# Performance work log

Measured on AMD Instinct MI355X. Metric: run time of the kernel, lower is better.

Reference implementation:

```python
import jax, jax.numpy as jnp
import numpy as np

B, S, R = 1, 512, 384
C_MSA, C_Z, C_HID, N_HEAD = 64, 128, 32, 8
INF = 1e8


def layer_norm(x, gamma, beta, eps=1e-5):
    mu = jnp.mean(x, axis=-1, keepdims=True)
    var = jnp.mean(jnp.square(x - mu), axis=-1, keepdims=True)
    return (x - mu) * jax.lax.rsqrt(var + eps) * gamma + beta


def setup_inputs() -> dict:
    key = jax.random.key(0)
    ks = jax.random.split(key, 8)
    hc = N_HEAD * C_HID
    return {
        "m": jax.random.normal(ks[0], (B, S, R, C_MSA), jnp.float32),
        "z": jax.random.normal(ks[1], (B, R, R, C_Z), jnp.float32),
        "msa_mask": jnp.ones((B, S, R), jnp.float32),
        "z_mask": jnp.ones((B, R, R), jnp.float32),
        "ln_m_g": jnp.ones((C_MSA,), jnp.float32),
        "ln_m_b": jnp.zeros((C_MSA,), jnp.float32),
        "w_v": jax.random.normal(ks[2], (C_MSA, hc), jnp.float32) / np.sqrt(C_MSA),
        "w_g": jax.random.normal(ks[3], (C_MSA, hc), jnp.float32) * 0.02,
        "ln_z_g": jnp.ones((C_Z,), jnp.float32),
        "ln_z_b": jnp.zeros((C_Z,), jnp.float32),
        "w_b": jax.random.normal(ks[4], (C_Z, N_HEAD), jnp.float32) / np.sqrt(C_Z),
        "w_o": jax.random.normal(ks[5], (hc, C_MSA), jnp.float32) * 0.02,
    }


def reference(m, z, msa_mask, z_mask, ln_m_g, ln_m_b, w_v, w_g, ln_z_g, ln_z_b, w_b, w_o):
    b_, s_, r_ = m.shape[0], m.shape[1], m.shape[2]
    m_ln = layer_norm(m, ln_m_g, ln_m_b)                       # [B,S,R,Cm]
    v = (m_ln @ w_v).reshape(b_, s_, r_, N_HEAD, C_HID)        # [B,S,R,H,C]
    g = jax.nn.sigmoid(m_ln @ w_g).reshape(b_, s_, r_, N_HEAD, C_HID)
    bias = layer_norm(z, ln_z_g, ln_z_b) @ w_b                 # [B,R,R,H]
    bias = bias + INF * (z_mask[..., None] - 1.0)
    v = v * msa_mask[..., None, None]
    w = jax.nn.softmax(bias, axis=2)                           # softmax over j
    # weighted average over residues j, then sigmoid gating
    o = g * jnp.einsum('bijh,bsjhc->bsihc', w, v)              # [B,S,R,H,C]
    o = o.reshape(b_, s_, r_, N_HEAD * C_HID)
    return o @ w_o                                             # [B,S,R,Cm]
```

## Files before the change

### kernel.cpp

```cpp
#include <hip/hip_runtime.h>
#include <math.h>

#define S_DIM 512
#define R_DIM 384
#define CM 64
#define CZ 128
#define NH 8
#define CH 32
#define HC 256

typedef unsigned short u16;
typedef __attribute__((ext_vector_type(8))) __bf16 bf16x8;
typedef __attribute__((ext_vector_type(4))) float f32x4;

static __device__ __forceinline__ u16 f2bf(float f) {
    unsigned int u = __float_as_uint(f);
    unsigned int r = (u + 0x7fffu + ((u >> 16) & 1u)) >> 16;
    return (u16)r;
}
static __device__ __forceinline__ float bf2f(u16 h) {
    return __uint_as_float(((unsigned int)h) << 16);
}
static __device__ __forceinline__ void split2(float f, u16& hi, u16& lo) {
    hi = f2bf(f);
    lo = f2bf(f - bf2f(hi));
}

__global__ __launch_bounds__(256) void kW_prep(
    const float* __restrict__ wv, const float* __restrict__ wg,
    u16* __restrict__ wvT_hi, u16* __restrict__ wvT_lo,
    u16* __restrict__ wgT_hi, u16* __restrict__ wgT_lo)
{
    const int idx = blockIdx.x * 256 + threadIdx.x;
    const int which = idx >> 14;
    const int r = idx & 16383;
    const int n = r >> 6, c = r & 63;
    if (which == 0) split2(wv[c * HC + n], wvT_hi[r], wvT_lo[r]);
    else            split2(wg[c * HC + n], wgT_hi[r], wgT_lo[r]);
}

__global__ __launch_bounds__(256) void kA1_bias(
    const float* __restrict__ z, const float* __restrict__ z_mask,
    const float* __restrict__ ln_z_g, const float* __restrict__ ln_z_b,
    const float* __restrict__ w_b, float* __restrict__ bias_ws)
{
    __shared__ float wb_s[CZ * NH];
    __shared__ float zn_s[4][CZ];
    const int tid = threadIdx.x, w = tid >> 6, lane = tid & 63;
    const int ridx = blockIdx.x * 4 + w;

    #pragma unroll
    for (int q = 0; q < 4; ++q) wb_s[tid * 4 + q] = w_b[tid * 4 + q];

    const float2 zz = *reinterpret_cast<const float2*>(
        z + (size_t)ridx * CZ + lane * 2);
    float s1 = zz.x + zz.y;
    float s2 = zz.x * zz.x + zz.y * zz.y;
    #pragma unroll
    for (int msk = 32; msk >= 1; msk >>= 1) {
        s1 += __shfl_xor(s1, msk);
        s2 += __shfl_xor(s2, msk);
    }
    const float mu   = s1 * (1.0f / CZ);
    const float var  = s2 * (1.0f / CZ) - mu * mu;
    const float rstd = rsqrtf(var + 1e-5f);
    const int c0 = lane * 2;
    zn_s[w][c0]     = (zz.x - mu) * rstd * ln_z_g[c0]     + ln_z_b[c0];
    zn_s[w][c0 + 1] = (zz.y - mu) * rstd * ln_z_g[c0 + 1] + ln_z_b[c0 + 1];
    __syncthreads();

    const int h = lane & 7, seg = lane >> 3;
    float acc = 0.f;
    #pragma unroll
    for (int t = 0; t < 16; ++t) {
        const int c = seg * 16 + t;
        acc += zn_s[w][c] * wb_s[c * NH + h];
    }
    acc += __shfl_xor(acc, 8);
    acc += __shfl_xor(acc, 16);
    acc += __shfl_xor(acc, 32);
    if (seg == 0)
        bias_ws[(size_t)h * R_DIM * R_DIM + ridx] =
            acc + 1e8f * (z_mask[ridx] - 1.0f);
}

__global__ __launch_bounds__(256) void kA2_softmax(
    const float* __restrict__ bias_ws, u16* __restrict__ w_soft)
{
    const int tid = threadIdx.x, w = tid >> 6, lane = tid & 63;
    const int row = blockIdx.x * 4 + w;
    const float* src = bias_ws + (size_t)row * R_DIM;
    float vals[6];
    float mx = -1e30f;
    #pragma unroll
    for (int u = 0; u < 6; ++u) {
        vals[u] = src[lane + u * 64];
        mx = fmaxf(mx, vals[u]);
    }
    #pragma unroll
    for (int msk = 32; msk >= 1; msk >>= 1) mx = fmaxf(mx, __shfl_xor(mx, msk));
    float sum = 0.f;
    #pragma unroll
    for (int u = 0; u < 6; ++u) { vals[u] = __expf(vals[u] - mx); sum += vals[u]; }
    #pragma unroll
    for (int msk = 32; msk >= 1; msk >>= 1) sum += __shfl_xor(sum, msk);
    const float inv = 1.0f / sum;
    u16* dst = w_soft + (size_t)row * R_DIM;
    #pragma unroll
    for (int u = 0; u < 6; ++u)
        dst[lane + u * 64] = f2bf(vals[u] * inv);
}

__global__ __launch_bounds__(256) void kB_mfma(
    const float* __restrict__ m_chunk, const float* __restrict__ mask_chunk,
    const float* __restrict__ ln_g, const float* __restrict__ ln_b,
    const u16* __restrict__ wvT_hi, const u16* __restrict__ wvT_lo,
    const u16* __restrict__ wgT_hi, const u16* __restrict__ wgT_lo,
    u16* __restrict__ Vt, u16* __restrict__ gbuf, int SCH)
{
    __shared__ __align__(16) u16 smem[4 * 128 * 72];
    u16* a_hi = smem;
    u16* a_lo = smem + 128 * 72;
    u16* b_hi = smem + 2 * 128 * 72;
    u16* b_lo = smem + 3 * 128 * 72;
    const int tid   = threadIdx.x;
    const int panel = blockIdx.x;
    const int si0   = blockIdx.y * 128;
    const int n0    = (panel & 1) * 128;
    const int lane  = tid & 63;
    const int w     = tid >> 6;
    const int wr    = (w >> 1) * 64, wc = (w & 1) * 64;

    {
        const int r = tid >> 1, half = tid & 1;
        const float* src = m_chunk + (size_t)(si0 + r) * CM + half * 32;
        float x[32];
        float s1 = 0.f, s2 = 0.f;
        #pragma unroll
        for (int e = 0; e < 8; ++e) {
            float4 v4 = *reinterpret_cast<const float4*>(src + e * 4);
            x[e*4+0] = v4.x; x[e*4+1] = v4.y; x[e*4+2] = v4.z; x[e*4+3] = v4.w;
            s1 += v4.x + v4.y + v4.z + v4.w;
            s2 += v4.x*v4.x + v4.y*v4.y + v4.z*v4.z + v4.w*v4.w;
        }
        s1 += __shfl_xor(s1, 1);
        s2 += __shfl_xor(s2, 1);
        const float mu   = s1 * (1.f / 64);
        const float var  = s2 * (1.f / 64) - mu * mu;
        const float rstd = rsqrtf(var + 1e-5f);
        #pragma unroll
        for (int e = 0; e < 8; ++e) {
            #pragma unroll
            for (int q = 0; q < 4; ++q) {
                const int c = half * 32 + e * 4 + q;
                const float v = (x[e*4+q] - mu) * rstd * ln_g[c] + ln_b[c];
                split2(v, a_hi[r * 72 + c], a_lo[r * 72 + c]);
            }
        }
    }
    {
        const u16* Wh = (panel < 2 ? wvT_hi : wgT_hi) + (size_t)n0 * 64;
        const u16* Wl = (panel < 2 ? wvT_lo : wgT_lo) + (size_t)n0 * 64;
        #pragma unroll
        for (int e = 0; e < 4; ++e) {
            const int c = e * 256 + tid;
            const int row = c >> 3, off = (c & 7) * 8;
            *reinterpret_cast<uint4*>(&b_hi[row * 72 + off]) =
                *reinterpret_cast<const uint4*>(Wh + row * 64 + off);
            *reinterpret_cast<uint4*>(&b_lo[row * 72 + off]) =
                *reinterpret_cast<const uint4*>(Wl + row * 64 + off);
        }
    }
    __syncthreads();

    f32x4 acc[4][4] = {};
    #pragma unroll
    for (int ks = 0; ks < 2; ++ks) {
        const int ko = ks * 32 + (lane >> 4) * 8;
        bf16x8 ah[4], al[4], bh[4], bl[4];
        #pragma unroll
        for (int mm = 0; mm < 4; ++mm) {
            const int base = (wr + mm * 16 + (lane & 15)) * 72 + ko;
            ah[mm] = *reinterpret_cast<const bf16x8*>(&a_hi[base]);
            al[mm] = *reinterpret_cast<const bf16x8*>(&a_lo[base]);
        }
        #pragma unroll
        for (int nn = 0; nn < 4; ++nn) {
            const int base = (wc + nn * 16 + (lane & 15)) * 72 + ko;
            bh[nn] = *reinterpret_cast<const bf16x8*>(&b_hi[base]);
            bl[nn] = *reinterpret_cast<const bf16x8*>(&b_lo[base]);
        }
        #pragma unroll
        for (int mm = 0; mm < 4; ++mm)
            #pragma unroll
            for (int nn = 0; nn < 4; ++nn) {
                acc[mm][nn] = __builtin_amdgcn_mfma_f32_16x16x32_bf16(
                    ah[mm], bh[nn], acc[mm][nn], 0, 0, 0);
                acc[mm][nn] = __builtin_amdgcn_mfma_f32_16x16x32_bf16(
                    al[mm], bh[nn], acc[mm][nn], 0, 0, 0);
                acc[mm][nn] = __builtin_amdgcn_mfma_f32_16x16x32_bf16(
                    ah[mm], bl[nn], acc[mm][nn], 0, 0, 0);
            }
    }

    __syncthreads();
    const int r4 = (lane >> 4) * 4, cl = lane & 15;
    if (panel < 2) {
        u16* T = smem;
        #pragma unroll
        for (int mm = 0; mm < 4; ++mm) {
            const int rowb = wr + mm * 16 + r4;
            const float4 mk = *reinterpret_cast<const float4*>(mask_chunk + si0 + rowb);
            #pragma unroll
            for (int nn = 0; nn < 4; ++nn) {
                const int n = wc + nn * 16 + cl;
                ushort4 pk;
                pk.x = f2bf(acc[mm][nn][0] * mk.x);
                pk.y = f2bf(acc[mm][nn][1] * mk.y);
                pk.z = f2bf(acc[mm][nn][2] * mk.z);
                pk.w = f2bf(acc[mm][nn][3] * mk.w);
                *reinterpret_cast<ushort4*>(&T[n * 136 + rowb]) = pk;
            }
        }
        __syncthreads();
        const int sc = si0 / R_DIM, j0 = si0 % R_DIM;
        const size_t Nn = (size_t)SCH * 32;
        #pragma unroll
        for (int e = 0; e < 8; ++e) {
            const int c = e * 256 + tid;
            const int n = c >> 4, part = c & 15;
            const int k = n0 + n;
            const int h = k >> 5, cc = k & 31;
            u16* dst = Vt + ((size_t)h * Nn + (size_t)sc * 32 + cc) * R_DIM
                         + j0 + part * 8;
            *reinterpret_cast<uint4*>(dst) =
                *reinterpret_cast<const uint4*>(&T[n * 136 + part * 8]);
        }
    } else {
        u16* T = smem;
        #pragma unroll
        for (int mm = 0; mm < 4; ++mm) {
            const int rowb = wr + mm * 16 + r4;
            #pragma unroll
            for (int nn = 0; nn < 4; ++nn) {
                const int n = wc + nn * 16 + cl;
                #pragma unroll
                for (int r = 0; r < 4; ++r)
                    T[(rowb + r) * 136 + n] =
                        f2bf(1.f / (1.f + __expf(-acc[mm][nn][r])));
            }
        }
        __syncthreads();
        #pragma unroll
        for (int e = 0; e < 8; ++e) {
            const int c = e * 256 + tid;
            const int row = c >> 4, part = c & 15;
            u16* dst = gbuf + (size_t)(si0 + row) * HC + n0 + part * 8;
            *reinterpret_cast<uint4*>(dst) =
                *reinterpret_cast<const uint4*>(&T[row * 136 + part * 8]);
        }
    }
}

__global__ __launch_bounds__(256) void kC_mfma(
    const u16* __restrict__ Wsoft, const u16* __restrict__ Vt,
    u16* __restrict__ o_pre, int SCH)
{
    constexpr int LDSP = 40;
    __shared__ __align__(16) u16 lds_a[128 * LDSP];
    __shared__ __align__(16) u16 lds_b[128 * LDSP];
    const int N   = SCH * 32;
    const int n0  = blockIdx.x * 128;
    const int i0  = blockIdx.y * 128;
    const int h   = blockIdx.z;
    const int tid = threadIdx.x;
    const int lane = tid & 63;
    const int w    = tid >> 6;
    const int wr   = (w >> 1) * 64;
    const int wc   = (w & 1) * 64;

    const u16* Wp = Wsoft + (size_t)h * R_DIM * R_DIM;
    const u16* Vp = Vt    + (size_t)h * N * R_DIM;

    f32x4 acc[4][4] = {};

    for (int k0 = 0; k0 < R_DIM; k0 += 32) {
        __syncthreads();
        #pragma unroll
        for (int rep = 0; rep < 2; ++rep) {
            const int c = rep * 256 + tid;
            const int row = c >> 2, q = c & 3;
            uint4 va = *reinterpret_cast<const uint4*>(
                Wp + (size_t)(i0 + row) * R_DIM + k0 + q * 8);
            *reinterpret_cast<uint4*>(&lds_a[row * LDSP + q * 8]) = va;
            uint4 vb = *reinterpret_cast<const uint4*>(
                Vp + (size_t)(n0 + row) * R_DIM + k0 + q * 8);
            *reinterpret_cast<uint4*>(&lds_b[row * LDSP + q * 8]) = vb;
        }
        __syncthreads();

        bf16x8 afrag[4], bfrag[4];
        #pragma unroll
        for (int mm = 0; mm < 4; ++mm) {
            const int row = wr + mm * 16 + (lane & 15);
            afrag[mm] = *reinterpret_cast<const bf16x8*>(
                &lds_a[row * LDSP + (lane >> 4) * 8]);
        }
        #pragma unroll
        for (int nn = 0; nn < 4; ++nn) {
            const int row = wc + nn * 16 + (lane & 15);
            bfrag[nn] = *reinterpret_cast<const bf16x8*>(
                &lds_b[row * LDSP + (lane >> 4) * 8]);
        }
        #pragma unroll
        for (int mm = 0; mm < 4; ++mm)
            #pragma unroll
            for (int nn = 0; nn < 4; ++nn)
                acc[mm][nn] = __builtin_amdgcn_mfma_f32_16x16x32_bf16(
                    afrag[mm], bfrag[nn], acc[mm][nn], 0, 0, 0);
    }

    const int r4 = (lane >> 4) * 4;
    const int cl = lane & 15;
    #pragma unroll
    for (int mm = 0; mm < 4; ++mm) {
        #pragma unroll
        for (int nn = 0; nn < 4; ++nn) {
            const int i = i0 + wr + mm * 16 + r4;
            const int n = n0 + wc + nn * 16 + cl;
            const int sc = n >> 5, cc = n & 31;
            u16* dst = &o_pre[((size_t)sc * R_DIM + i) * HC + h * 32 + cc];
            #pragma unroll
            for (int r = 0; r < 4; ++r)
                dst[(size_t)r * HC] = f2bf(acc[mm][nn][r]);
        }
    }
}

__global__ __launch_bounds__(256) void kD_out(
    const u16* __restrict__ gbuf, const u16* __restrict__ o_pre,
    const float* __restrict__ w_o, float* __restrict__ out_chunk, int SCH)
{
    __shared__ float A[128 * 65];
    __shared__ float Bt[64 * 64];
    const int si0 = blockIdx.x * 128;
    const int tid = threadIdx.x;
    const int tx  = tid & 15, ty = tid >> 4;
    float acc[8][4] = {};

    for (int k0 = 0; k0 < HC; k0 += 64) {
        {
            const int r = tid >> 1, half = tid & 1;
            const size_t base = (size_t)(si0 + r) * HC + k0 + half * 32;
            float* dst = &A[r * 65 + half * 32];
            #pragma unroll
            for (int e = 0; e < 4; ++e) {
                uint4 gv = *reinterpret_cast<const uint4*>(gbuf + base + e * 8);
                uint4 ov = *reinterpret_cast<const uint4*>(o_pre + base + e * 8);
                const u16* ga = (const u16*)&gv;
                const u16* oa = (const u16*)&ov;
                #pragma unroll
                for (int q = 0; q < 8; ++q)
                    dst[e * 8 + q] = bf2f(ga[q]) * bf2f(oa[q]);
            }
        }
        {
            const int kk = tid >> 2, q = tid & 3;
            #pragma unroll
            for (int e = 0; e < 4; ++e) {
                float4 v4 = *reinterpret_cast<const float4*>(
                    w_o + (size_t)(k0 + kk) * CM + q * 16 + e * 4);
                *reinterpret_cast<float4*>(&Bt[kk * 64 + q * 16 + e * 4]) = v4;
            }
        }
        __syncthreads();
        #pragma unroll 8
        for (int kk = 0; kk < 64; ++kk) {
            float4 b = *reinterpret_cast<float4*>(&Bt[kk * 64 + tx * 4]);
            #pragma unroll
            for (int e = 0; e < 8; ++e) {
                float a = A[(ty * 8 + e) * 65 + kk];
                acc[e][0] += a * b.x; acc[e][1] += a * b.y;
                acc[e][2] += a * b.z; acc[e][3] += a * b.w;
            }
        }
        __syncthreads();
    }
    #pragma unroll
    for (int e = 0; e < 8; ++e) {
        *reinterpret_cast<float4*>(
            &out_chunk[(size_t)(si0 + ty * 8 + e) * CM + tx * 4]) =
            make_float4(acc[e][0], acc[e][1], acc[e][2], acc[e][3]);
    }
}

extern "C" void kernel_launch(void* const* d_in, const int* in_sizes, int n_in,
                              void* d_out, int out_size, void* d_ws, size_t ws_size,
                              hipStream_t stream)
{
    const float* m        = (const float*)d_in[0];
    const float* z        = (const float*)d_in[1];
    const float* msa_mask = (const float*)d_in[2];
    const float* z_mask   = (const float*)d_in[3];
    const float* ln_m_g   = (const float*)d_in[4];
    const float* ln_m_b   = (const float*)d_in[5];
    const float* w_v      = (const float*)d_in[6];
    const float* w_g      = (const float*)d_in[7];
    const float* ln_z_g   = (const float*)d_in[8];
    const float* ln_z_b   = (const float*)d_in[9];
    const float* w_b      = (const float*)d_in[10];
    const float* w_o      = (const float*)d_in[11];
    float* out = (float*)d_out;

    const size_t wsoft_bytes = (size_t)NH * R_DIM * R_DIM * 2;
    const size_t bias_bytes  = (size_t)NH * R_DIM * R_DIM * 4;
    const size_t wts_bytes   = 4 * 16384 * 2;
    const size_t per_sch = (size_t)R_DIM * HC * (2 + 2 + 2);
    int SCH = 256;
    while (SCH > 4 &&
           wsoft_bytes + bias_bytes + wts_bytes + (size_t)SCH * per_sch > ws_size)
        SCH >>= 1;

    char* p = (char*)d_ws;
    u16* w_soft   = (u16*)p; p += wsoft_bytes;
    float* biasws = (float*)p; p += bias_bytes;
    u16* wvT_hi   = (u16*)p; p += 16384 * 2;
    u16* wvT_lo   = (u16*)p; p += 16384 * 2;
    u16* wgT_hi   = (u16*)p; p += 16384 * 2;
    u16* wgT_lo   = (u16*)p; p += 16384 * 2;
    u16* Vt       = (u16*)p; p += (size_t)SCH * 32 * NH * R_DIM * 2;
    u16* gbuf     = (u16*)p; p += (size_t)SCH * R_DIM * HC * 2;
    u16* obuf     = (u16*)p;

    kW_prep<<<128, 256, 0, stream>>>(w_v, w_g, wvT_hi, wvT_lo, wgT_hi, wgT_lo);
    kA1_bias<<<R_DIM * R_DIM / 4, 256, 0, stream>>>(
        z, z_mask, ln_z_g, ln_z_b, w_b, biasws);
    kA2_softmax<<<NH * R_DIM / 4, 256, 0, stream>>>(biasws, w_soft);

    for (int s0 = 0; s0 < S_DIM; s0 += SCH) {
        kB_mfma<<<dim3(4, SCH * 3), 256, 0, stream>>>(
            m + (size_t)s0 * R_DIM * CM, msa_mask + (size_t)s0 * R_DIM,
            ln_m_g, ln_m_b, wvT_hi, wvT_lo, wgT_hi, wgT_lo, Vt, gbuf, SCH);
        kC_mfma<<<dim3(SCH / 4, 3, NH), 256, 0, stream>>>(w_soft, Vt, obuf, SCH);
        kD_out<<<dim3(SCH * 3), 256, 0, stream>>>(gbuf, obuf, w_o,
                                                  out + (size_t)s0 * R_DIM * CM, SCH);
    }
}
```

Before: 361.8 us.

## Compute z-bias projection with split-bf16 MFMA over 128-row tiles

Replaces the per-row scalar LayerNorm plus dot-product bias kernel with a tiled kernel that handles 128 rows of z per block. Normalized z and a padded transposed w_b are split into hi/lo bf16 pairs in shared memory, and the projection runs on MFMA with three products to keep near-fp32 accuracy. Results are transposed through LDS and written as coalesced float4 stores. This removes the per-row w_b reload and the shuffle reductions, at the cost of padding 8 heads to 16 and higher register and LDS use per block.

New measurement: 328.1 us. 1.1x faster.

```diff
diff --git a/kernel.cpp b/kernel.cpp
--- a/kernel.cpp
+++ b/kernel.cpp
@@ -28,60 +28,122 @@
 
 __global__ __launch_bounds__(256) void kW_prep(
     const float* __restrict__ wv, const float* __restrict__ wg,
+    const float* __restrict__ wb,
     u16* __restrict__ wvT_hi, u16* __restrict__ wvT_lo,
-    u16* __restrict__ wgT_hi, u16* __restrict__ wgT_lo)
+    u16* __restrict__ wgT_hi, u16* __restrict__ wgT_lo,
+    u16* __restrict__ wbT_hi, u16* __restrict__ wbT_lo)
 {
     const int idx = blockIdx.x * 256 + threadIdx.x;
-    const int which = idx >> 14;
-    const int r = idx & 16383;
-    const int n = r >> 6, c = r & 63;
-    if (which == 0) split2(wv[c * HC + n], wvT_hi[r], wvT_lo[r]);
-    else            split2(wg[c * HC + n], wgT_hi[r], wgT_lo[r]);
+    if (idx < 16384) {
+        const int n = idx >> 6, c = idx & 63;
+        split2(wv[c * HC + n], wvT_hi[idx], wvT_lo[idx]);
+    } else if (idx < 32768) {
+        const int r = idx - 16384;
+        const int n = r >> 6, c = r & 63;
+        split2(wg[c * HC + n], wgT_hi[r], wgT_lo[r]);
+    } else if (idx < 34816) {
+        const int r = idx - 32768;
+        const int n = r >> 7, c = r & 127;
+        split2(n < NH ? wb[c * NH + n] : 0.f, wbT_hi[r], wbT_lo[r]);
+    }
 }
 
 __global__ __launch_bounds__(256) void kA1_bias(
     const float* __restrict__ z, const float* __restrict__ z_mask,
     const float* __restrict__ ln_z_g, const float* __restrict__ ln_z_b,
-    const float* __restrict__ w_b, float* __restrict__ bias_ws)
-{
-    __shared__ float wb_s[CZ * NH];
-    __shared__ float zn_s[4][CZ];
-    const int tid = threadIdx.x, w = tid >> 6, lane = tid & 63;
-    const int ridx = blockIdx.x * 4 + w;
-
-    #pragma unroll
-    for (int q = 0; q < 4; ++q) wb_s[tid * 4 + q] = w_b[tid * 4 + q];
-
-    const float2 zz = *reinterpret_cast<const float2*>(
-        z + (size_t)ridx * CZ + lane * 2);
-    float s1 = zz.x + zz.y;
-    float s2 = zz.x * zz.x + zz.y * zz.y;
-    #pragma unroll
-    for (int msk = 32; msk >= 1; msk >>= 1) {
-        s1 += __shfl_xor(s1, msk);
-        s2 += __shfl_xor(s2, msk);
-    }
-    const float mu   = s1 * (1.0f / CZ);
-    const float var  = s2 * (1.0f / CZ) - mu * mu;
-    const float rstd = rsqrtf(var + 1e-5f);
-    const int c0 = lane * 2;
-    zn_s[w][c0]     = (zz.x - mu) * rstd * ln_z_g[c0]     + ln_z_b[c0];
-    zn_s[w][c0 + 1] = (zz.y - mu) * rstd * ln_z_g[c0 + 1] + ln_z_b[c0 + 1];
+    const u16* __restrict__ wbT_hi, const u16* __restrict__ wbT_lo,
+    float* __restrict__ bias_ws)
+{
+    __shared__ __align__(16) u16 a_hi[128 * 136];
+    __shared__ __align__(16) u16 a_lo[128 * 136];
+    __shared__ __align__(16) u16 b_hi[16 * 136];
+    __shared__ __align__(16) u16 b_lo[16 * 136];
+    const int tid  = threadIdx.x;
+    const int lane = tid & 63, w = tid >> 6;
+    const int row0 = blockIdx.x * 128;
+
+    {
+        const int r = tid >> 1, half = tid & 1;
+        const float* src = z + (size_t)(row0 + r) * CZ + half * 64;
+        float x[64];
+        float s1 = 0.f, s2 = 0.f;
+        #pragma unroll
+        for (int e = 0; e < 16; ++e) {
+            float4 v4 = *reinterpret_cast<const float4*>(src + e * 4);
+            x[e*4+0] = v4.x; x[e*4+1] = v4.y; x[e*4+2] = v4.z; x[e*4+3] = v4.w;
+            s1 += v4.x + v4.y + v4.z + v4.w;
+            s2 += v4.x*v4.x + v4.y*v4.y + v4.z*v4.z + v4.w*v4.w;
+        }
+        s1 += __shfl_xor(s1, 1);
+        s2 += __shfl_xor(s2, 1);
+        const float mu   = s1 * (1.f / CZ);
+        const float var  = s2 * (1.f / CZ) - mu * mu;
+        const float rstd = rsqrtf(var + 1e-5f);
+        #pragma unroll
+        for (int e = 0; e < 16; ++e) {
+            float4 g4 = *reinterpret_cast<const float4*>(ln_z_g + half * 64 + e * 4);
+            float4 b4 = *reinterpret_cast<const float4*>(ln_z_b + half * 64 + e * 4);
+            const int c = half * 64 + e * 4;
+            split2((x[e*4+0] - mu) * rstd * g4.x + b4.x,
+                   a_hi[r * 136 + c + 0], a_lo[r * 136 + c + 0]);
+            split2((x[e*4+1] - mu) * rstd * g4.y + b4.y,
+                   a_hi[r * 136 + c + 1], a_lo[r * 136 + c + 1]);
+            split2((x[e*4+2] - mu) * rstd * g4.z + b4.z,
+                   a_hi[r * 136 + c + 2], a_lo[r * 136 + c + 2]);
+            split2((x[e*4+3] - mu) * rstd * g4.w + b4.w,
+                   a_hi[r * 136 + c + 3], a_lo[r * 136 + c + 3]);
+        }
+    }
+    {
+        const int row = tid >> 4, off = (tid & 15) * 8;
+        *reinterpret_cast<uint4*>(&b_hi[row * 136 + off]) =
+            *reinterpret_cast<const uint4*>(wbT_hi + row * 128 + off);
+        *reinterpret_cast<uint4*>(&b_lo[row * 136 + off]) =
+            *reinterpret_cast<const uint4*>(wbT_lo + row * 128 + off);
+    }
     __syncthreads();
 
-    const int h = lane & 7, seg = lane >> 3;
-    float acc = 0.f;
-    #pragma unroll
-    for (int t = 0; t < 16; ++t) {
-        const int c = seg * 16 + t;
-        acc += zn_s[w][c] * wb_s[c * NH + h];
-    }
-    acc += __shfl_xor(acc, 8);
-    acc += __shfl_xor(acc, 16);
-    acc += __shfl_xor(acc, 32);
-    if (seg == 0)
-        bias_ws[(size_t)h * R_DIM * R_DIM + ridx] =
-            acc + 1e8f * (z_mask[ridx] - 1.0f);
+    const int wr = w * 32;
+    f32x4 acc[2] = {};
+    #pragma unroll
+    for (int ks = 0; ks < 4; ++ks) {
+        const int ko = ks * 32 + (lane >> 4) * 8;
+        bf16x8 bh = *reinterpret_cast<const bf16x8*>(&b_hi[(lane & 15) * 136 + ko]);
+        bf16x8 bl = *reinterpret_cast<const bf16x8*>(&b_lo[(lane & 15) * 136 + ko]);
+        #pragma unroll
+        for (int mm = 0; mm < 2; ++mm) {
+            const int base = (wr + mm * 16 + (lane & 15)) * 136 + ko;
+            bf16x8 ah = *reinterpret_cast<const bf16x8*>(&a_hi[base]);
+            bf16x8 al = *reinterpret_cast<const bf16x8*>(&a_lo[base]);
+            acc[mm] = __builtin_amdgcn_mfma_f32_16x16x32_bf16(ah, bh, acc[mm], 0, 0, 0);
+            acc[mm] = __builtin_amdgcn_mfma_f32_16x16x32_bf16(al, bh, acc[mm], 0, 0, 0);
+            acc[mm] = __builtin_amdgcn_mfma_f32_16x16x32_bf16(ah, bl, acc[mm], 0, 0, 0);
+        }
+    }
+
+    __syncthreads();
+    float* T = reinterpret_cast<float*>(a_hi);
+    const int cl = lane & 15, r4 = (lane >> 4) * 4;
+    #pragma unroll
+    for (int mm = 0; mm < 2; ++mm) {
+        if (cl < NH) {
+            #pragma unroll
+            for (int r = 0; r < 4; ++r)
+                T[cl * 132 + wr + mm * 16 + r4 + r] = acc[mm][r];
+        }
+    }
+    __syncthreads();
+    {
+        const int h = tid >> 5, q = (tid & 31) * 4;
+        float4 v  = *reinterpret_cast<const float4*>(&T[h * 132 + q]);
+        float4 mk = *reinterpret_cast<const float4*>(z_mask + row0 + q);
+        v.x += 1e8f * (mk.x - 1.f);
+        v.y += 1e8f * (mk.y - 1.f);
+        v.z += 1e8f * (mk.z - 1.f);
+        v.w += 1e8f * (mk.w - 1.f);
+        *reinterpret_cast<float4*>(
+            &bias_ws[(size_t)h * R_DIM * R_DIM + row0 + q]) = v;
+    }
 }
 
 __global__ __launch_bounds__(256) void kA2_softmax(
@@ -414,7 +476,7 @@
 
     const size_t wsoft_bytes = (size_t)NH * R_DIM * R_DIM * 2;
     const size_t bias_bytes  = (size_t)NH * R_DIM * R_DIM * 4;
-    const size_t wts_bytes   = 4 * 16384 * 2;
+    const size_t wts_bytes   = 4 * 16384 * 2 + 2 * 2048 * 2;
     const size_t per_sch = (size_t)R_DIM * HC * (2 + 2 + 2);
     int SCH = 256;
     while (SCH > 4 &&
@@ -428,13 +490,16 @@
     u16* wvT_lo   = (u16*)p; p += 16384 * 2;
     u16* wgT_hi   = (u16*)p; p += 16384 * 2;
     u16* wgT_lo   = (u16*)p; p += 16384 * 2;
+    u16* wbT_hi   = (u16*)p; p += 2048 * 2;
+    u16* wbT_lo   = (u16*)p; p += 2048 * 2;
     u16* Vt       = (u16*)p; p += (size_t)SCH * 32 * NH * R_DIM * 2;
     u16* gbuf     = (u16*)p; p += (size_t)SCH * R_DIM * HC * 2;
     u16* obuf     = (u16*)p;
 
-    kW_prep<<<128, 256, 0, stream>>>(w_v, w_g, wvT_hi, wvT_lo, wgT_hi, wgT_lo);
-    kA1_bias<<<R_DIM * R_DIM / 4, 256, 0, stream>>>(
-        z, z_mask, ln_z_g, ln_z_b, w_b, biasws);
+    kW_prep<<<136, 256, 0, stream>>>(w_v, w_g, w_b, wvT_hi, wvT_lo,
+                                     wgT_hi, wgT_lo, wbT_hi, wbT_lo);
+    kA1_bias<<<R_DIM * R_DIM / 128, 256, 0, stream>>>(
+        z, z_mask, ln_z_g, ln_z_b, wbT_hi, wbT_lo, biasws);
     kA2_softmax<<<NH * R_DIM / 4, 256, 0, stream>>>(biasws, w_soft);
 
     for (int s0 = 0; s0 < S_DIM; s0 += SCH) {
```
